# Optimization experiments

Measured on AMD Instinct MI355X. Metric: run time of the kernel, lower is better.

Reference implementation:

```python
import jax, jax.numpy as jnp
import numpy as np

COMMITMENT_COST = 0.25

def setup_inputs() -> dict:
    key = jax.random.key(0)
    k1, k2 = jax.random.split(key)
    z = jax.random.normal(k1, (8, 2048, 768), dtype=jnp.float32)
    # codebook initialized uniform(-1/K, 1/K) in the original; use same scale
    K = 2048
    emb = jax.random.uniform(k2, (K, 768), dtype=jnp.float32, minval=-1.0 / K, maxval=1.0 / K)
    return {"z": z, "emb": emb}

def reference(z, emb):
    B, S, D = z.shape
    z_flat = z.reshape(-1, D)                                   # [N, D]
    # squared-euclidean distances via expansion: ||z||^2 + ||e||^2 - 2 z e^T
    distances = (
        jnp.sum(z_flat * z_flat, axis=1, keepdims=True)
        + jnp.sum(emb * emb, axis=1)
        - 2.0 * jnp.matmul(z_flat, emb.T)
    )                                                           # [N, K]
    ids_flat = jnp.argmin(distances, axis=1)                    # [N]
    z_q = emb[ids_flat].reshape(z.shape)                        # gather + reshape
    concept_ids = ids_flat.reshape(B, S)
    # training path with use_ema=True: codebook_loss = 0, commitment term only.
    # NOTE: original (faithfully) computes mse(z.detach(), z_q) — grad flows to z_q.
    commitment_loss = jnp.mean((jax.lax.stop_gradient(z) - z_q) ** 2)
    vq_loss = COMMITMENT_COST * commitment_loss
    # straight-through estimator
    z_q_st = z + jax.lax.stop_gradient(z_q - z)
    return z_q_st, concept_ids, vq_loss
```

## Files before the change

kernel.cpp:

```cpp
#include <hip/hip_runtime.h>
#include <float.h>

typedef unsigned short ushort_t;
typedef unsigned int uint_t;

#define NROWS 16384
#define DDIM  768
#define KCODES 2048
#define MARGIN 8e-4f

__device__ __forceinline__ ushort_t f2bf(float x) {
    uint_t u = __float_as_uint(x);
    uint_t r = (u + 0x7fffu + ((u >> 16) & 1u)) >> 16;
    return (ushort_t)r;
}

__device__ __forceinline__ uint_t fenc(float f) {
    uint_t u = __float_as_uint(f);
    return (u & 0x80000000u) ? ~u : (u | 0x80000000u);
}
__device__ __forceinline__ float fdec(uint_t k) {
    uint_t u = (k & 0x80000000u) ? (k ^ 0x80000000u) : ~k;
    return __uint_as_float(u);
}

typedef __attribute__((ext_vector_type(8))) short bf16x8;
typedef __attribute__((ext_vector_type(4))) float f32x4;

__global__ void prep2_kernel(const float* __restrict__ emb, float* __restrict__ ee,
                             ushort_t* __restrict__ Eh, float* __restrict__ out_loss) {
    const int c = blockIdx.x, t = threadIdx.x;
    if (c == 0 && t == 0) out_loss[0] = 0.f;
    const float* e = emb + (size_t)c * DDIM;
    float s = 0.f;
    for (int i = t; i < DDIM; i += 256) { float v = e[i]; s += v * v; }
    for (int off = 32; off; off >>= 1) s += __shfl_down(s, off);
    __shared__ float red[4];
    if ((t & 63) == 0) red[t >> 6] = s;
    __syncthreads();
    if (t == 0) ee[c] = red[0] + red[1] + red[2] + red[3];
    if (t < 192) {
        const float4 v = ((const float4*)e)[t];
        ushort4 h;
        h.x = f2bf(v.x); h.y = f2bf(v.y); h.z = f2bf(v.z); h.w = f2bf(v.w);
        ((ushort4*)(Eh + (size_t)c * DDIM))[t] = h;
    }
}

#define WGROWS   64
#define CHUNK    128
#define NCHUNKS  16
#define KSTEPS   12
#define CAP      16
#define B_OFF    98304
#define RMIN_OFF 131072
#define RCNT_OFF 131328
#define SVAL_OFF 131584
#define SIDX_OFF 135680
#define LRED_OFF 139776
#define SMEM_BYTES 139808

__global__ __launch_bounds__(512, 2)
void fused_kernel(const float* __restrict__ z, const float* __restrict__ emb,
                  const ushort_t* __restrict__ Eh, const float* __restrict__ ee,
                  float* __restrict__ ids_f32, float* __restrict__ out0,
                  float* __restrict__ out_loss) {
    __shared__ __align__(16) char smem[SMEM_BYTES];
    uint_t* rowminU = (uint_t*)(smem + RMIN_OFF);
    int*    rcnt    = (int*)(smem + RCNT_OFF);
    float (*sval)[CAP] = (float(*)[CAP])(smem + SVAL_OFF);
    int   (*sidx)[CAP] = (int(*)[CAP])(smem + SIDX_OFF);
    float*  lred    = (float*)(smem + LRED_OFF);

    const int t = threadIdx.x;
    const int w = t >> 6, l = t & 63;
    const int row0 = blockIdx.x * WGROWS;

    if (t < 64) { rowminU[t] = 0xFFFFFFFFu; rcnt[t] = 0; }

    float zzr[8];
    #pragma unroll
    for (int rr = 0; rr < 8; ++rr) {
        const int row = row0 + w * 8 + rr;
        const float* zr = z + (size_t)row * DDIM;
        float s = 0.f;
        #pragma unroll
        for (int k = 0; k < 12; ++k) { const float v = zr[l + 64 * k]; s += v * v; }
        for (int off = 32; off; off >>= 1) s += __shfl_down(s, off);
        zzr[rr] = __shfl(s, 0);
    }

    {
        const int ar = t >> 3;
        const int as = t & 7;
        const float4* zr4 = (const float4*)(z + (size_t)(row0 + ar) * DDIM);
        char* abase = smem + ar * 1536;
        const int rx = (ar & 7) << 4;
        #pragma unroll
        for (int j = 0; j < 12; ++j) {
            const int slot = as + 8 * j;
            const float4 v0 = zr4[2 * slot];
            const float4 v1 = zr4[2 * slot + 1];
            ushort4 h0, h1;
            h0.x = f2bf(v0.x); h0.y = f2bf(v0.y); h0.z = f2bf(v0.z); h0.w = f2bf(v0.w);
            h1.x = f2bf(v1.x); h1.y = f2bf(v1.y); h1.z = f2bf(v1.z); h1.w = f2bf(v1.w);
            char* p = abase + ((slot << 4) ^ rx);
            *(ushort4*)p = h0;
            *(ushort4*)(p + 8) = h1;
        }
    }

    const int brow_l  = l >> 3;
    const int srcslot = (l & 7) ^ brow_l;
    const ushort_t* gB[2];
    #pragma unroll
    for (int q = 0; q < 2; ++q) {
        const int grow = q * 64 + w * 8 + brow_l;
        gB[q] = Eh + (size_t)grow * DDIM + srcslot * 8;
    }

    const int wr = w >> 2, wc = w & 3;
    const int g = l >> 4, lr = l & 15;
    int aoff[2][2], boff[2][2];
    #pragma unroll
    for (int mi = 0; mi < 2; ++mi) {
        const int arow = wr * 32 + mi * 16 + lr;
        #pragma unroll
        for (int kf = 0; kf < 2; ++kf)
            aoff[mi][kf] = arow * 1536 + ((((kf << 2) + g) << 4) ^ ((arow & 7) << 4));
    }
    #pragma unroll
    for (int ni = 0; ni < 2; ++ni) {
        const int brow = wc * 32 + ni * 16 + lr;
        #pragma unroll
        for (int kf = 0; kf < 2; ++kf)
            boff[ni][kf] = brow * 128 + ((((kf << 2) + g) << 4) ^ ((brow & 7) << 4));
    }

    int cur = 0;
    #pragma unroll
    for (int q = 0; q < 2; ++q) {
        __builtin_amdgcn_global_load_lds(
            (const __attribute__((address_space(1))) void*)gB[q],
            (__attribute__((address_space(3))) void*)(smem + B_OFF + q * 8192 + w * 1024),
            16, 0, 0);
        gB[q] += 64;
    }
    __syncthreads();

    for (int c = 0; c < NCHUNKS; ++c) {
        const int c0 = c * CHUNK;
        f32x4 acc[2][2];
        #pragma unroll
        for (int mi = 0; mi < 2; ++mi)
            #pragma unroll
            for (int ni = 0; ni < 2; ++ni) acc[mi][ni] = (f32x4){0.f, 0.f, 0.f, 0.f};

        for (int s = 0; s < KSTEPS; ++s) {
            if (!(c == NCHUNKS - 1 && s == KSTEPS - 1)) {
                const int nb = B_OFF + (cur ^ 1) * 16384 + w * 1024;
                #pragma unroll
                for (int q = 0; q < 2; ++q)
                    __builtin_amdgcn_global_load_lds(
                        (const __attribute__((address_space(1))) void*)gB[q],
                        (__attribute__((address_space(3))) void*)(smem + nb + q * 8192),
                        16, 0, 0);
                const int adv = (s == KSTEPS - 2) ? (64 + 127 * 768) : 64;
                gB[0] += adv; gB[1] += adv;
            }
            const char* Bb = smem + B_OFF + cur * 16384;
            bf16x8 af[2][2], bfv[2][2];
            #pragma unroll
            for (int mi = 0; mi < 2; ++mi)
                #pragma unroll
                for (int kf = 0; kf < 2; ++kf)
                    af[mi][kf] = *(const bf16x8*)(smem + aoff[mi][kf] + s * 128);
            #pragma unroll
            for (int ni = 0; ni < 2; ++ni)
                #pragma unroll
                for (int kf = 0; kf < 2; ++kf)
                    bfv[ni][kf] = *(const bf16x8*)(Bb + boff[ni][kf]);
            #pragma unroll
            for (int kf = 0; kf < 2; ++kf)
                #pragma unroll
                for (int mi = 0; mi < 2; ++mi)
                    #pragma unroll
                    for (int ni = 0; ni < 2; ++ni)
                        acc[mi][ni] = __builtin_amdgcn_mfma_f32_16x16x32_bf16(
                            af[mi][kf], bfv[ni][kf], acc[mi][ni], 0, 0, 0);
            __syncthreads();
            cur ^= 1;
        }

        float ecv[2];
        #pragma unroll
        for (int ni = 0; ni < 2; ++ni) ecv[ni] = ee[c0 + wc * 32 + ni * 16 + lr];
        float dv[2][2][4];
        #pragma unroll
        for (int mi = 0; mi < 2; ++mi)
            #pragma unroll
            for (int ni = 0; ni < 2; ++ni)
                #pragma unroll
                for (int r = 0; r < 4; ++r)
                    dv[mi][ni][r] = ecv[ni] - 2.0f * acc[mi][ni][r];

        #pragma unroll
        for (int mi = 0; mi < 2; ++mi)
            #pragma unroll
            for (int r = 0; r < 4; ++r) {
                float v = fminf(dv[mi][0][r], dv[mi][1][r]);
                v = fminf(v, __shfl_xor(v, 1));
                v = fminf(v, __shfl_xor(v, 2));
                v = fminf(v, __shfl_xor(v, 4));
                v = fminf(v, __shfl_xor(v, 8));
                if (lr == 0) atomicMin(&rowminU[wr * 32 + mi * 16 + g * 4 + r], fenc(v));
            }
        __syncthreads();
        #pragma unroll
        for (int mi = 0; mi < 2; ++mi)
            #pragma unroll
            for (int r = 0; r < 4; ++r) {
                const int lrow = wr * 32 + mi * 16 + g * 4 + r;
                const float lim = fdec(rowminU[lrow]) + MARGIN;
                #pragma unroll
                for (int ni = 0; ni < 2; ++ni) {
                    const float vv = dv[mi][ni][r];
                    if (vv <= lim) {
                        const int p = atomicAdd(&rcnt[lrow], 1);
                        if (p < CAP) {
                            sval[lrow][p] = vv;
                            sidx[lrow][p] = c0 + wc * 32 + ni * 16 + lr;
                        }
                    }
                }
            }
    }
    __syncthreads();

    float wloss = 0.f;
    for (int rr = 0; rr < 8; ++rr) {
        const int lrow = w * 8 + rr;
        const int row = row0 + lrow;
        const float T = fdec(rowminU[lrow]) + MARGIN;
        const int n = rcnt[lrow] < CAP ? rcnt[lrow] : CAP;
        float val = FLT_MAX; int idx = 0x7fffffff;
        if (l < n) { val = sval[lrow][l]; idx = sidx[lrow][l]; }
        unsigned long long m = __ballot(val <= T);
        const float* zr = z + (size_t)row * DDIM;
        float bestd = FLT_MAX; int besti = 0x7fffffff;
        while (m) {
            const int j = __ffsll(m) - 1; m &= m - 1;
            const int cand = __shfl(idx, j);
            const float* er = emb + (size_t)cand * DDIM;
            float p = 0.f;
            #pragma unroll
            for (int k = 0; k < 12; ++k) p += zr[l + 64 * k] * er[l + 64 * k];
            for (int off = 32; off; off >>= 1) p += __shfl_down(p, off);
            if (l == 0) {
                const float t1 = zzr[rr] + ee[cand];
                const float d  = t1 - 2.0f * p;
                if (d < bestd || (d == bestd && cand < besti)) { bestd = d; besti = cand; }
            }
        }
        const int bi = __shfl(besti, 0);
        if (l == 0) ids_f32[row] = (float)bi;

        const float4* zr4 = (const float4*)zr;
        const float4* er4 = (const float4*)(emb + (size_t)bi * DDIM);
        float4* o4 = (float4*)(out0 + (size_t)row * DDIM);
        float s = 0.f;
        #pragma unroll
        for (int j2 = 0; j2 < 3; ++j2) {
            const int i4 = l + 64 * j2;
            const float4 zv = zr4[i4];
            const float4 ev = er4[i4];
            float4 o;
            o.x = zv.x + (ev.x - zv.x); o.y = zv.y + (ev.y - zv.y);
            o.z = zv.z + (ev.z - zv.z); o.w = zv.w + (ev.w - zv.w);
            o4[i4] = o;
            const float dx = zv.x - ev.x, dy = zv.y - ev.y;
            const float dz = zv.z - ev.z, dw = zv.w - ev.w;
            s += dx * dx + dy * dy + dz * dz + dw * dw;
        }
        for (int off = 32; off; off >>= 1) s += __shfl_down(s, off);
        if (l == 0) wloss += s;
    }
    if (l == 0) lred[w] = wloss;
    __syncthreads();
    if (t == 0) {
        float tot = 0.f;
        #pragma unroll
        for (int i = 0; i < 8; ++i) tot += lred[i];
        atomicAdd(out_loss, tot * (0.25f / (float)((size_t)NROWS * DDIM)));
    }
}

__global__ void ee_kernel(const float* __restrict__ emb, float* __restrict__ ee) {
    int c = blockIdx.x;
    const float* e = emb + (size_t)c * DDIM;
    int t = threadIdx.x;
    float s = 0.f;
    for (int i = t; i < DDIM; i += 256) { float v = e[i]; s += v * v; }
    for (int off = 32; off; off >>= 1) s += __shfl_down(s, off);
    __shared__ float red[4];
    if ((t & 63) == 0) red[t >> 6] = s;
    __syncthreads();
    if (t == 0) ee[c] = red[0] + red[1] + red[2] + red[3];
}

__global__ void zz_kernel(const float* __restrict__ z, float* __restrict__ zz) {
    const int t = threadIdx.x;
    const int row = blockIdx.x * 4 + (t >> 6);
    const int lane = t & 63;
    const float* zr = z + (size_t)row * DDIM;
    float s = 0.f;
    for (int i = lane; i < DDIM; i += 64) { float v = zr[i]; s += v * v; }
    for (int off = 32; off; off >>= 1) s += __shfl_down(s, off);
    if (lane == 0) zz[row] = s;
}

#define BM 32
#define BN 128
#define BKS 32
#define SPLITC 2
#define CODES_PER_BLOCK (KCODES / SPLITC)
#define NCHUNK (CODES_PER_BLOCK / BN)
#define NSTAGE (DDIM / BKS)
#define APADR 33
#define BPADC 132

__global__ __launch_bounds__(256)
void argmin_kernel(const float* __restrict__ z, const float* __restrict__ emb,
                   const float* __restrict__ ee, const float* __restrict__ zz,
                   float* __restrict__ pval, int* __restrict__ pidx) {
    __shared__ float Af[BKS][APADR];
    __shared__ float Bf[BKS][BPADC];
    __shared__ float cval[BM][33];
    __shared__ int   cidx[BM][33];
    __shared__ float zzs[BM];
    const int t = threadIdx.x;
    const int part = blockIdx.x & (SPLITC - 1);
    const int rb = blockIdx.x >> 1;
    const int row0 = rb * BM;
    const int cbase = part * CODES_PER_BLOCK;
    const int tx = t & 31, ty = t >> 5;
    const int sr = t >> 3;
    const int sk = 4 * (t & 7);
    if (t < BM) zzs[t] = zz[row0 + t];
    float bv[4]; int bi[4];
    #pragma unroll
    for (int i = 0; i < 4; ++i) { bv[i] = FLT_MAX; bi[i] = 0x7fffffff; }
    const float* zt = z + (size_t)(row0 + sr) * DDIM;
    for (int chunk = 0; chunk < NCHUNK; ++chunk) {
        const int c0 = cbase + chunk * BN;
        const float* ebase = emb + (size_t)(c0 + sr) * DDIM;
        float acc[4][4];
        #pragma unroll
        for (int i = 0; i < 4; ++i)
            #pragma unroll
            for (int j = 0; j < 4; ++j) acc[i][j] = 0.f;
        float4 pa = *(const float4*)&zt[sk];
        float4 pb[4];
        #pragma unroll
        for (int m = 0; m < 4; ++m) pb[m] = *(const float4*)&ebase[(size_t)(32 * m) * DDIM + sk];
        for (int s = 0; s < NSTAGE; ++s) {
            __syncthreads();
            Af[sk + 0][sr] = pa.x; Af[sk + 1][sr] = pa.y;
            Af[sk + 2][sr] = pa.z; Af[sk + 3][sr] = pa.w;
            #pragma unroll
            for (int m = 0; m < 4; ++m) {
                Bf[sk + 0][sr + 32 * m] = pb[m].x;
                Bf[sk + 1][sr + 32 * m] = pb[m].y;
                Bf[sk + 2][sr + 32 * m] = pb[m].z;
                Bf[sk + 3][sr + 32 * m] = pb[m].w;
            }
            __syncthreads();
            if (s + 1 < NSTAGE) {
                const int k1 = (s + 1) * BKS + sk;
                pa = *(const float4*)&zt[k1];
                #pragma unroll
                for (int m = 0; m < 4; ++m)
                    pb[m] = *(const float4*)&ebase[(size_t)(32 * m) * DDIM + k1];
            }
            #pragma unroll
            for (int kk = 0; kk < BKS; ++kk) {
                const float4 a4 = *(const float4*)&Af[kk][4 * ty];
                const float4 b4 = *(const float4*)&Bf[kk][4 * tx];
                const float aa[4] = {a4.x, a4.y, a4.z, a4.w};
                const float bb[4] = {b4.x, b4.y, b4.z, b4.w};
                #pragma unroll
                for (int i = 0; i < 4; ++i)
                    #pragma unroll
                    for (int j = 0; j < 4; ++j) acc[i][j] += aa[i] * bb[j];
            }
        }
        const float4 e4 = *(const float4*)&ee[c0 + 4 * tx];
        const float eev[4] = {e4.x, e4.y, e4.z, e4.w};
        #pragma unroll
        for (int i = 0; i < 4; ++i) {
            const float zzr = zzs[4 * ty + i];
            #pragma unroll
            for (int j = 0; j < 4; ++j) {
                const int code = c0 + 4 * tx + j;
                const float t1 = zzr + eev[j];
                const float d  = t1 - 2.0f * acc[i][j];
                if (d < bv[i] || (d == bv[i] && code < bi[i])) { bv[i] = d; bi[i] = code; }
            }
        }
    }
    __syncthreads();
    #pragma unroll
    for (int i = 0; i < 4; ++i) { cval[4 * ty + i][tx] = bv[i]; cidx[4 * ty + i][tx] = bi[i]; }
    __syncthreads();
    if (t < BM) {
        float v = FLT_MAX; int id = 0x7fffffff;
        #pragma unroll
        for (int x = 0; x < 32; ++x) {
            const float cv = cval[t][x]; const int ci = cidx[t][x];
            if (cv < v || (cv == v && ci < id)) { v = cv; id = ci; }
        }
        pval[part * NROWS + row0 + t] = v;
        pidx[part * NROWS + row0 + t] = id;
    }
}

__global__ void combine_kernel(const float* __restrict__ pval, const int* __restrict__ pidx,
                               float* __restrict__ ids_f32) {
    const int r = blockIdx.x * 256 + threadIdx.x;
    float v = pval[r];           int id = pidx[r];
    const float v1 = pval[NROWS + r]; const int i1 = pidx[NROWS + r];
    if (v1 < v || (v1 == v && i1 < id)) { v = v1; id = i1; }
    ids_f32[r] = (float)id;
}

__global__ __launch_bounds__(256)
void gather_kernel(const float* __restrict__ z, const float* __restrict__ emb,
                   const float* __restrict__ ids_f32, float* __restrict__ out0,
                   float* __restrict__ part) {
    const int b = blockIdx.x;
    const int t = threadIdx.x;
    const int rl = t >> 4, c = t & 15;
    __shared__ int ids[16];
    if (t < 16) ids[t] = (int)ids_f32[b * 16 + t];
    __syncthreads();
    const int row = b * 16 + rl;
    const float4* zr = (const float4*)(z + (size_t)row * DDIM);
    float4* orow = (float4*)(out0 + (size_t)row * DDIM);
    const float4* er = (const float4*)(emb + (size_t)ids[rl] * DDIM);
    float s = 0.f;
    #pragma unroll
    for (int j = 0; j < 12; ++j) {
        const int i4 = c + 16 * j;
        const float4 zv = zr[i4];
        const float4 ev = er[i4];
        float4 o;
        o.x = zv.x + (ev.x - zv.x); o.y = zv.y + (ev.y - zv.y);
        o.z = zv.z + (ev.z - zv.z); o.w = zv.w + (ev.w - zv.w);
        orow[i4] = o;
        float dx = zv.x - ev.x, dy = zv.y - ev.y, dz = zv.z - ev.z, dw = zv.w - ev.w;
        s += dx * dx + dy * dy + dz * dz + dw * dw;
    }
    for (int off = 32; off; off >>= 1) s += __shfl_down(s, off);
    __shared__ float red[4];
    if ((t & 63) == 0) red[t >> 6] = s;
    __syncthreads();
    if (t == 0) part[b] = red[0] + red[1] + red[2] + red[3];
}

__global__ void loss_kernel(const float* __restrict__ part, float* __restrict__ out_loss) {
    const int t = threadIdx.x;
    double s = 0.0;
    for (int i = t; i < 1024; i += 256) s += (double)part[i];
    for (int off = 32; off; off >>= 1) s += __shfl_down(s, off);
    __shared__ double red[4];
    if ((t & 63) == 0) red[t >> 6] = s;
    __syncthreads();
    if (t == 0) {
        const double total = red[0] + red[1] + red[2] + red[3];
        out_loss[0] = (float)(0.25 * (total / (double)((size_t)NROWS * DDIM)));
    }
}

#define EE_OFF   0
#define ZZ_OFF   8192
#define EH_OFF   73728
#define WS_NEED  (EH_OFF + (size_t)KCODES * DDIM * 2)
#define PART_OFF 73728
#define PV_OFF   81920

extern "C" void kernel_launch(void* const* d_in, const int* in_sizes, int n_in,
                              void* d_out, int out_size, void* d_ws, size_t ws_size,
                              hipStream_t stream) {
    const float* z   = (const float*)d_in[0];
    const float* emb = (const float*)d_in[1];

    float* out0     = (float*)d_out;
    float* out_ids  = out0 + (size_t)NROWS * DDIM;
    float* out_loss = out_ids + NROWS;

    char* ws = (char*)d_ws;
    float* ee   = (float*)(ws + EE_OFF);
    float* zzws = (float*)(ws + ZZ_OFF);

    if (ws_size >= WS_NEED) {
        ushort_t* Eh = (ushort_t*)(ws + EH_OFF);
        prep2_kernel<<<KCODES, 256, 0, stream>>>(emb, ee, Eh, out_loss);
        fused_kernel<<<NROWS / WGROWS, 512, 0, stream>>>(z, emb, Eh, ee,
                                                         out_ids, out0, out_loss);
    } else {
        float* part = (float*)(ws + PART_OFF);
        float* pval = (float*)(ws + PV_OFF);
        int*   pidx = (int*)(ws + PV_OFF + 131072);
        ee_kernel<<<KCODES, 256, 0, stream>>>(emb, ee);
        zz_kernel<<<NROWS / 4, 256, 0, stream>>>(z, zzws);
        argmin_kernel<<<(NROWS / BM) * SPLITC, 256, 0, stream>>>(z, emb, ee, zzws, pval, pidx);
        combine_kernel<<<NROWS / 256, 256, 0, stream>>>(pval, pidx, out_ids);
        gather_kernel<<<NROWS / 16, 256, 0, stream>>>(z, emb, out_ids, out0, part);
        loss_kernel<<<1, 256, 0, stream>>>(part, out_loss);
    }
}
```

Measured before the change: 250.9 us.

## Restructure fused VQ kernel to stream A per k-step with larger per-wave tiles

Measured after the change: 278.1 us. 1.11x slower.

```diff
diff --git a/kernel.cpp b/kernel.cpp
--- a/kernel.cpp
+++ b/kernel.cpp
@@ -25,7 +25,10 @@
 }
 
 typedef __attribute__((ext_vector_type(8))) short bf16x8;
+typedef __attribute__((ext_vector_type(8))) unsigned short ushort8;
 typedef __attribute__((ext_vector_type(4))) float f32x4;
+
+__device__ __forceinline__ int swz(int r) { return (r & 3) ^ ((r >> 2) & 3); }
 
 __global__ void prep2_kernel(const float* __restrict__ emb, float* __restrict__ ee,
                              ushort_t* __restrict__ Eh, float* __restrict__ out_loss) {
@@ -47,25 +50,25 @@
     }
 }
 
-#define WGROWS   64
-#define CHUNK    128
-#define NCHUNKS  16
-#define KSTEPS   12
-#define CAP      16
-#define B_OFF    98304
-#define RMIN_OFF 131072
-#define RCNT_OFF 131328
-#define SVAL_OFF 131584
-#define SIDX_OFF 135680
-#define LRED_OFF 139776
-#define SMEM_BYTES 139808
-
-__global__ __launch_bounds__(512, 2)
-void fused_kernel(const float* __restrict__ z, const float* __restrict__ emb,
-                  const ushort_t* __restrict__ Eh, const float* __restrict__ ee,
-                  float* __restrict__ ids_f32, float* __restrict__ out0,
-                  float* __restrict__ out_loss) {
-    __shared__ __align__(16) char smem[SMEM_BYTES];
+#define R      64
+#define CCH    512
+#define NCH    4
+#define KST    24
+#define CAP    16
+#define B_OFF    4096
+#define RMIN_OFF 36864
+#define RCNT_OFF 37120
+#define SVAL_OFF 37376
+#define SIDX_OFF 41472
+#define LRED_OFF 45568
+#define SMEM_SZ  45600
+
+__global__ __launch_bounds__(256, 2)
+void fused2_kernel(const float* __restrict__ z, const float* __restrict__ emb,
+                   const ushort_t* __restrict__ Eh, const float* __restrict__ ee,
+                   float* __restrict__ ids_f32, float* __restrict__ out0,
+                   float* __restrict__ out_loss) {
+    __shared__ __align__(16) char smem[SMEM_SZ];
     uint_t* rowminU = (uint_t*)(smem + RMIN_OFF);
     int*    rcnt    = (int*)(smem + RCNT_OFF);
     float (*sval)[CAP] = (float(*)[CAP])(smem + SVAL_OFF);
@@ -74,162 +77,113 @@
 
     const int t = threadIdx.x;
     const int w = t >> 6, l = t & 63;
-    const int row0 = blockIdx.x * WGROWS;
+    const int row0 = blockIdx.x * R;
 
     if (t < 64) { rowminU[t] = 0xFFFFFFFFu; rcnt[t] = 0; }
 
-    float zzr[8];
+    const int arow = t >> 2, acs = t & 3;
+    const float* zA = z + (size_t)(row0 + arow) * DDIM + acs * 8;
+    char* aw = smem + (arow << 6) + ((acs ^ swz(arow)) << 4);
+
+    const int sri = l >> 2, slot = l & 3;
+    const int swzs = swz(sri);
+    const int brow = w * 128 + sri;
+    const uint_t lB = B_OFF + (uint_t)(w * 8192);
+
+    const int g = l >> 4, lr = l & 15;
+    int aoff[4], boff[8];
     #pragma unroll
-    for (int rr = 0; rr < 8; ++rr) {
-        const int row = row0 + w * 8 + rr;
-        const float* zr = z + (size_t)row * DDIM;
-        float s = 0.f;
-        #pragma unroll
-        for (int k = 0; k < 12; ++k) { const float v = zr[l + 64 * k]; s += v * v; }
-        for (int off = 32; off; off >>= 1) s += __shfl_down(s, off);
-        zzr[rr] = __shfl(s, 0);
-    }
-
-    {
-        const int ar = t >> 3;
-        const int as = t & 7;
-        const float4* zr4 = (const float4*)(z + (size_t)(row0 + ar) * DDIM);
-        char* abase = smem + ar * 1536;
-        const int rx = (ar & 7) << 4;
-        #pragma unroll
-        for (int j = 0; j < 12; ++j) {
-            const int slot = as + 8 * j;
-            const float4 v0 = zr4[2 * slot];
-            const float4 v1 = zr4[2 * slot + 1];
-            ushort4 h0, h1;
-            h0.x = f2bf(v0.x); h0.y = f2bf(v0.y); h0.z = f2bf(v0.z); h0.w = f2bf(v0.w);
-            h1.x = f2bf(v1.x); h1.y = f2bf(v1.y); h1.z = f2bf(v1.z); h1.w = f2bf(v1.w);
-            char* p = abase + ((slot << 4) ^ rx);
-            *(ushort4*)p = h0;
-            *(ushort4*)(p + 8) = h1;
-        }
-    }
-
-    const int brow_l  = l >> 3;
-    const int srcslot = (l & 7) ^ brow_l;
-    const ushort_t* gB[2];
+    for (int mi = 0; mi < 4; ++mi) {
+        const int r = mi * 16 + lr;
+        aoff[mi] = (r << 6) + ((g ^ swz(r)) << 4);
+    }
     #pragma unroll
-    for (int q = 0; q < 2; ++q) {
-        const int grow = q * 64 + w * 8 + brow_l;
-        gB[q] = Eh + (size_t)grow * DDIM + srcslot * 8;
-    }
-
-    const int wr = w >> 2, wc = w & 3;
-    const int g = l >> 4, lr = l & 15;
-    int aoff[2][2], boff[2][2];
-    #pragma unroll
-    for (int mi = 0; mi < 2; ++mi) {
-        const int arow = wr * 32 + mi * 16 + lr;
-        #pragma unroll
-        for (int kf = 0; kf < 2; ++kf)
-            aoff[mi][kf] = arow * 1536 + ((((kf << 2) + g) << 4) ^ ((arow & 7) << 4));
-    }
-    #pragma unroll
-    for (int ni = 0; ni < 2; ++ni) {
-        const int brow = wc * 32 + ni * 16 + lr;
-        #pragma unroll
-        for (int kf = 0; kf < 2; ++kf)
-            boff[ni][kf] = brow * 128 + ((((kf << 2) + g) << 4) ^ ((brow & 7) << 4));
-    }
-
-    int cur = 0;
-    #pragma unroll
-    for (int q = 0; q < 2; ++q) {
-        __builtin_amdgcn_global_load_lds(
-            (const __attribute__((address_space(1))) void*)gB[q],
-            (__attribute__((address_space(3))) void*)(smem + B_OFF + q * 8192 + w * 1024),
-            16, 0, 0);
-        gB[q] += 64;
-    }
-    __syncthreads();
-
-    for (int c = 0; c < NCHUNKS; ++c) {
-        const int c0 = c * CHUNK;
-        f32x4 acc[2][2];
-        #pragma unroll
-        for (int mi = 0; mi < 2; ++mi)
-            #pragma unroll
-            for (int ni = 0; ni < 2; ++ni) acc[mi][ni] = (f32x4){0.f, 0.f, 0.f, 0.f};
-
-        for (int s = 0; s < KSTEPS; ++s) {
-            if (!(c == NCHUNKS - 1 && s == KSTEPS - 1)) {
-                const int nb = B_OFF + (cur ^ 1) * 16384 + w * 1024;
-                #pragma unroll
-                for (int q = 0; q < 2; ++q)
-                    __builtin_amdgcn_global_load_lds(
-                        (const __attribute__((address_space(1))) void*)gB[q],
-                        (__attribute__((address_space(3))) void*)(smem + nb + q * 8192),
-                        16, 0, 0);
-                const int adv = (s == KSTEPS - 2) ? (64 + 127 * 768) : 64;
-                gB[0] += adv; gB[1] += adv;
-            }
-            const char* Bb = smem + B_OFF + cur * 16384;
-            bf16x8 af[2][2], bfv[2][2];
-            #pragma unroll
-            for (int mi = 0; mi < 2; ++mi)
-                #pragma unroll
-                for (int kf = 0; kf < 2; ++kf)
-                    af[mi][kf] = *(const bf16x8*)(smem + aoff[mi][kf] + s * 128);
-            #pragma unroll
-            for (int ni = 0; ni < 2; ++ni)
-                #pragma unroll
-                for (int kf = 0; kf < 2; ++kf)
-                    bfv[ni][kf] = *(const bf16x8*)(Bb + boff[ni][kf]);
-            #pragma unroll
-            for (int kf = 0; kf < 2; ++kf)
-                #pragma unroll
-                for (int mi = 0; mi < 2; ++mi)
-                    #pragma unroll
-                    for (int ni = 0; ni < 2; ++ni)
-                        acc[mi][ni] = __builtin_amdgcn_mfma_f32_16x16x32_bf16(
-                            af[mi][kf], bfv[ni][kf], acc[mi][ni], 0, 0, 0);
+    for (int ni = 0; ni < 8; ++ni) {
+        const int rb = w * 128 + ni * 16 + lr;
+        boff[ni] = B_OFF + (rb << 6) + ((g ^ swz(rb)) << 4);
+    }
+
+    f32x4 acc[4][8];
+    for (int c = 0; c < NCH; ++c) {
+        const int c0 = c * CCH;
+        #pragma unroll
+        for (int mi = 0; mi < 4; ++mi)
+            #pragma unroll
+            for (int ni = 0; ni < 8; ++ni) acc[mi][ni] = (f32x4){0.f, 0.f, 0.f, 0.f};
+
+        const ushort_t* gB = Eh + (size_t)(c0 + brow) * DDIM + ((slot ^ swzs) << 3);
+
+        for (int s = 0; s < KST; ++s) {
             __syncthreads();
-            cur ^= 1;
-        }
-
-        float ecv[2];
-        #pragma unroll
-        for (int ni = 0; ni < 2; ++ni) ecv[ni] = ee[c0 + wc * 32 + ni * 16 + lr];
-        float dv[2][2][4];
-        #pragma unroll
-        for (int mi = 0; mi < 2; ++mi)
-            #pragma unroll
-            for (int ni = 0; ni < 2; ++ni)
+            #pragma unroll
+            for (int q = 0; q < 8; ++q)
+                __builtin_amdgcn_global_load_lds(
+                    (const __attribute__((address_space(1))) void*)(gB + q * (16 * DDIM)),
+                    (__attribute__((address_space(3))) void*)(smem + lB + q * 1024),
+                    16, 0, 0);
+            {
+                const float4 v0 = *(const float4*)(zA + 32 * s);
+                const float4 v1 = *(const float4*)(zA + 32 * s + 4);
+                ushort8 h;
+                h[0] = f2bf(v0.x); h[1] = f2bf(v0.y); h[2] = f2bf(v0.z); h[3] = f2bf(v0.w);
+                h[4] = f2bf(v1.x); h[5] = f2bf(v1.y); h[6] = f2bf(v1.z); h[7] = f2bf(v1.w);
+                *(ushort8*)aw = h;
+            }
+            gB += 32;
+            __syncthreads();
+
+            bf16x8 af[4], bfr[8];
+            #pragma unroll
+            for (int mi = 0; mi < 4; ++mi) af[mi] = *(const bf16x8*)(smem + aoff[mi]);
+            #pragma unroll
+            for (int ni = 0; ni < 8; ++ni) bfr[ni] = *(const bf16x8*)(smem + boff[ni]);
+            #pragma unroll
+            for (int mi = 0; mi < 4; ++mi)
+                #pragma unroll
+                for (int ni = 0; ni < 8; ++ni)
+                    acc[mi][ni] = __builtin_amdgcn_mfma_f32_16x16x32_bf16(
+                        af[mi], bfr[ni], acc[mi][ni], 0, 0, 0);
+        }
+
+        float ecv[8];
+        #pragma unroll
+        for (int ni = 0; ni < 8; ++ni) ecv[ni] = ee[c0 + w * 128 + ni * 16 + lr];
+        #pragma unroll
+        for (int mi = 0; mi < 4; ++mi)
+            #pragma unroll
+            for (int ni = 0; ni < 8; ++ni)
                 #pragma unroll
                 for (int r = 0; r < 4; ++r)
-                    dv[mi][ni][r] = ecv[ni] - 2.0f * acc[mi][ni][r];
-
-        #pragma unroll
-        for (int mi = 0; mi < 2; ++mi)
+                    acc[mi][ni][r] = ecv[ni] - 2.0f * acc[mi][ni][r];
+
+        #pragma unroll
+        for (int mi = 0; mi < 4; ++mi)
             #pragma unroll
             for (int r = 0; r < 4; ++r) {
-                float v = fminf(dv[mi][0][r], dv[mi][1][r]);
+                float v = acc[mi][0][r];
+                #pragma unroll
+                for (int ni = 1; ni < 8; ++ni) v = fminf(v, acc[mi][ni][r]);
                 v = fminf(v, __shfl_xor(v, 1));
                 v = fminf(v, __shfl_xor(v, 2));
                 v = fminf(v, __shfl_xor(v, 4));
                 v = fminf(v, __shfl_xor(v, 8));
-                if (lr == 0) atomicMin(&rowminU[wr * 32 + mi * 16 + g * 4 + r], fenc(v));
+                if (lr == 0) atomicMin(&rowminU[mi * 16 + g * 4 + r], fenc(v));
             }
         __syncthreads();
         #pragma unroll
-        for (int mi = 0; mi < 2; ++mi)
+        for (int mi = 0; mi < 4; ++mi)
             #pragma unroll
             for (int r = 0; r < 4; ++r) {
-                const int lrow = wr * 32 + mi * 16 + g * 4 + r;
+                const int lrow = mi * 16 + g * 4 + r;
                 const float lim = fdec(rowminU[lrow]) + MARGIN;
                 #pragma unroll
-                for (int ni = 0; ni < 2; ++ni) {
-                    const float vv = dv[mi][ni][r];
+                for (int ni = 0; ni < 8; ++ni) {
+                    const float vv = acc[mi][ni][r];
                     if (vv <= lim) {
                         const int p = atomicAdd(&rcnt[lrow], 1);
                         if (p < CAP) {
                             sval[lrow][p] = vv;
-                            sidx[lrow][p] = c0 + wc * 32 + ni * 16 + lr;
+                            sidx[lrow][p] = c0 + w * 128 + ni * 16 + lr;
                         }
                     }
                 }
@@ -238,15 +192,23 @@
     __syncthreads();
 
     float wloss = 0.f;
-    for (int rr = 0; rr < 8; ++rr) {
-        const int lrow = w * 8 + rr;
+    for (int rr = 0; rr < 16; ++rr) {
+        const int lrow = w * 16 + rr;
         const int row = row0 + lrow;
+        const float* zr = z + (size_t)row * DDIM;
+
+        float szz = 0.f;
+        #pragma unroll
+        for (int k = 0; k < 12; ++k) { const float v = zr[l + 64 * k]; szz += v * v; }
+        for (int off = 32; off; off >>= 1) szz += __shfl_down(szz, off);
+        const float zzr = __shfl(szz, 0);
+
         const float T = fdec(rowminU[lrow]) + MARGIN;
         const int n = rcnt[lrow] < CAP ? rcnt[lrow] : CAP;
         float val = FLT_MAX; int idx = 0x7fffffff;
         if (l < n) { val = sval[lrow][l]; idx = sidx[lrow][l]; }
         unsigned long long m = __ballot(val <= T);
-        const float* zr = z + (size_t)row * DDIM;
+
         float bestd = FLT_MAX; int besti = 0x7fffffff;
         while (m) {
             const int j = __ffsll(m) - 1; m &= m - 1;
@@ -257,7 +219,7 @@
             for (int k = 0; k < 12; ++k) p += zr[l + 64 * k] * er[l + 64 * k];
             for (int off = 32; off; off >>= 1) p += __shfl_down(p, off);
             if (l == 0) {
-                const float t1 = zzr[rr] + ee[cand];
+                const float t1 = zzr + ee[cand];
                 const float d  = t1 - 2.0f * p;
                 if (d < bestd || (d == bestd && cand < besti)) { bestd = d; besti = cand; }
             }
@@ -288,9 +250,7 @@
     if (l == 0) lred[w] = wloss;
     __syncthreads();
     if (t == 0) {
-        float tot = 0.f;
-        #pragma unroll
-        for (int i = 0; i < 8; ++i) tot += lred[i];
+        float tot = lred[0] + lred[1] + lred[2] + lred[3];
         atomicAdd(out_loss, tot * (0.25f / (float)((size_t)NROWS * DDIM)));
     }
 }
@@ -505,8 +465,8 @@
     if (ws_size >= WS_NEED) {
         ushort_t* Eh = (ushort_t*)(ws + EH_OFF);
         prep2_kernel<<<KCODES, 256, 0, stream>>>(emb, ee, Eh, out_loss);
-        fused_kernel<<<NROWS / WGROWS, 512, 0, stream>>>(z, emb, Eh, ee,
-                                                         out_ids, out0, out_loss);
+        fused2_kernel<<<NROWS / R, 256, 0, stream>>>(z, emb, Eh, ee,
+                                                     out_ids, out0, out_loss);
     } else {
         float* part = (float*)(ws + PART_OFF);
         float* pval = (float*)(ws + PV_OFF);
```
